# Performance work log

Measured on AMD Instinct MI355X. Metric: run time of the kernel, lower is better.

## Reference

```python
import jax, jax.numpy as jnp
import numpy as np

NOISE_STD = 0.05
ALPHA = 0.2
B, T, I, H, O = 64, 1000, 16, 512, 8


def setup_inputs() -> dict:
    key = jax.random.key(0)
    ks = jax.random.split(key, 5)
    x = jax.random.normal(ks[0], (B, T, I), dtype=jnp.float32)
    noise = jax.random.normal(ks[1], (B, T, H), dtype=jnp.float32)
    # parameter init mirrors torch: wi ~ N(0,1), wrec ~ N(0, rho/sqrt(H)), wo ~ N(0, 1/H)
    wi = jax.random.normal(ks[2], (I, H), dtype=jnp.float32)
    si = jnp.ones((I,), dtype=jnp.float32)
    wrec = jax.random.normal(ks[3], (H, H), dtype=jnp.float32) * (1.0 / np.sqrt(H))
    wo = jax.random.normal(ks[4], (H, O), dtype=jnp.float32) * (1.0 / H)
    so = jnp.ones((O,), dtype=jnp.float32)
    h0 = jnp.zeros((H,), dtype=jnp.float32)
    return {"x": x, "noise": noise, "wi": wi, "si": si, "wrec": wrec,
            "wo": wo, "so": so, "h0": h0}


def reference(x, noise, wi, si, wrec, wo, so, h0):
    # proxy params: wi_full = (wi.T * si).T ; wo_full = wo * so
    wi_full = si[:, None] * wi            # (I, H)
    wo_full = wo * so                      # (H, O)
    # input projection is time-parallel; hoist out of the scan
    x_proj = jnp.einsum('bti,ih->bth', x, wi_full)  # (B, T, H)

    def step(h, inp):
        xp, nz = inp                       # (B, H) each
        r = jnp.tanh(h)
        h_new = h + NOISE_STD * nz + ALPHA * (-h + r @ wrec.T + xp)
        out_t = jnp.tanh(h_new) @ wo_full  # (B, O)
        return h_new, out_t

    h_init = jnp.broadcast_to(h0, (x.shape[0], h0.shape[0]))
    _, out = jax.lax.scan(step, h_init,
                          (jnp.swapaxes(x_proj, 0, 1), jnp.swapaxes(noise, 0, 1)))
    return jnp.swapaxes(out, 0, 1)         # (B, T, O)
```

## Files before the change

### kernel.cpp

```cpp
#include <hip/hip_runtime.h>

#define BB 64
#define TT 1000
#define II 16
#define HH 512
#define OO 8
#define NOISE_STD 0.05f
#define ALPHA 0.2f

#define NGROUPS 32
#define BPG 2
#define NSLABS 8
#define JS 64
#define NTHREADS 512
#define NBLOCKS (NGROUPS * NSLABS)


__global__ void __launch_bounds__(NTHREADS, 1) rnn_kernel(
    const float* __restrict__ x, const float* __restrict__ noise,
    const float* __restrict__ wi, const float* __restrict__ si,
    const float* __restrict__ wrec, const float* __restrict__ wo,
    const float* __restrict__ so, const float* __restrict__ h0,
    float* __restrict__ out, unsigned long long* rtag)
{
    __shared__ __align__(16) float rlds[2][BPG][HH];
    __shared__ __align__(16) float zpart[NSLABS][BPG][JS];
    __shared__ __align__(16) float xpbuf[2][BPG][JS];

    const int tid  = threadIdx.x;
    const int lane = tid & 63;
    const int wid  = tid >> 6;

    const int xcd  = blockIdx.x & 7;
    const int bidx = blockIdx.x >> 3;
    const int grp  = xcd * 4 + (bidx >> 3);
    const int slab = bidx & 7;
    const int gb   = grp * BPG;
    const int j0   = slab * JS;

    float w_reg[64];
    {
        const float4* wrow = (const float4*)(wrec + (size_t)(j0 + lane) * HH + wid * 64);
        #pragma unroll
        for (int c = 0; c < 16; ++c) {
            float4 v = wrow[c];
            w_reg[4*c+0] = v.x; w_reg[4*c+1] = v.y;
            w_reg[4*c+2] = v.z; w_reg[4*c+3] = v.w;
        }
    }

    float hreg = 0.f;
    if (wid < BPG) hreg = h0[j0 + lane];

    float wiF_r[16];
    if (wid >= 6) {
        #pragma unroll
        for (int i = 0; i < 16; ++i) wiF_r[i] = si[i] * wi[i * HH + j0 + lane];
    }
    float wo_r[8][8];
    if (wid == 4 || wid == 5) {
        float so_[8];
        #pragma unroll
        for (int o = 0; o < 8; ++o) so_[o] = so[o];
        #pragma unroll
        for (int m = 0; m < 8; ++m) {
            const float4* wrow = (const float4*)(wo + (size_t)(lane + 64 * m) * OO);
            float4 wa = wrow[0], wb2 = wrow[1];
            wo_r[m][0] = wa.x  * so_[0]; wo_r[m][1] = wa.y  * so_[1];
            wo_r[m][2] = wa.z  * so_[2]; wo_r[m][3] = wa.w  * so_[3];
            wo_r[m][4] = wb2.x * so_[4]; wo_r[m][5] = wb2.y * so_[5];
            wo_r[m][6] = wb2.z * so_[6]; wo_r[m][7] = wb2.w * so_[7];
        }
    }

    {
        float rv = tanhf(h0[tid]);
        rlds[0][0][tid] = rv;
        rlds[0][1][tid] = rv;
    }
    if (wid >= 6) {
        const int b = wid - 6;
        const float4* xb = (const float4*)(x + ((size_t)(gb + b) * TT + 0) * II);
        float4 x0 = xb[0], x1 = xb[1], x2 = xb[2], x3 = xb[3];
        xpbuf[0][b][lane] =
              x0.x*wiF_r[0]  + x0.y*wiF_r[1]  + x0.z*wiF_r[2]  + x0.w*wiF_r[3]
            + x1.x*wiF_r[4]  + x1.y*wiF_r[5]  + x1.z*wiF_r[6]  + x1.w*wiF_r[7]
            + x2.x*wiF_r[8]  + x2.y*wiF_r[9]  + x2.z*wiF_r[10] + x2.w*wiF_r[11]
            + x3.x*wiF_r[12] + x3.y*wiF_r[13] + x3.z*wiF_r[14] + x3.w*wiF_r[15];
    }
    __syncthreads();

    for (int t = 0; t < TT; ++t) {
        const int par = t & 1;
        const int nxt = (t + 1) & 1;

        float nz = 0.f;
        if (wid < BPG)
            nz = noise[((size_t)(gb + wid) * TT + t) * HH + j0 + lane];

        if (t > 0 && wid != slab) {
            const unsigned long long* s0 =
                rtag + (size_t)par * (BB * HH) + (size_t)gb * HH + wid * 64 + lane;
            unsigned long long v0, v1;
            const unsigned int tg = (unsigned int)t;
            do {
                v0 = __hip_atomic_load(s0,      __ATOMIC_RELAXED, __HIP_MEMORY_SCOPE_AGENT);
                v1 = __hip_atomic_load(s0 + HH, __ATOMIC_RELAXED, __HIP_MEMORY_SCOPE_AGENT);
            } while ((unsigned int)(v0 >> 32) != tg || (unsigned int)(v1 >> 32) != tg);
            rlds[par][0][wid * 64 + lane] = __uint_as_float((unsigned int)v0);
            rlds[par][1][wid * 64 + lane] = __uint_as_float((unsigned int)v1);
        }

        float a0 = 0.f, a1 = 0.f;
        {
            const float4* r0p = (const float4*)&rlds[par][0][wid * 64];
            const float4* r1p = (const float4*)&rlds[par][1][wid * 64];
            #pragma unroll
            for (int c = 0; c < 16; ++c) {
                float4 r0 = r0p[c];
                float4 r1 = r1p[c];
                a0 += w_reg[4*c+0]*r0.x + w_reg[4*c+1]*r0.y
                    + w_reg[4*c+2]*r0.z + w_reg[4*c+3]*r0.w;
                a1 += w_reg[4*c+0]*r1.x + w_reg[4*c+1]*r1.y
                    + w_reg[4*c+2]*r1.z + w_reg[4*c+3]*r1.w;
            }
        }
        zpart[wid][0][lane] = a0;
        zpart[wid][1][lane] = a1;
        __syncthreads();

        if (wid < BPG) {
            float z = 0.f;
            #pragma unroll
            for (int k8 = 0; k8 < 8; ++k8) z += zpart[k8][wid][lane];
            float xp = xpbuf[par][wid][lane];
            float hn = hreg + NOISE_STD * nz + ALPHA * (z + xp - hreg);
            hreg = hn;
            float rnew = tanhf(hn);
            unsigned long long pv =
                ((unsigned long long)(unsigned int)(t + 1) << 32)
              | (unsigned long long)__float_as_uint(rnew);
            __hip_atomic_store(rtag + (size_t)nxt * (BB * HH)
                                    + (size_t)(gb + wid) * HH + j0 + lane,
                               pv, __ATOMIC_RELAXED, __HIP_MEMORY_SCOPE_AGENT);
            rlds[nxt][wid][j0 + lane] = rnew;
        } else if (wid == 4 || wid == 5) {
            const int b = wid - 4;
            if (t > 0) {
                float acc0=0.f,acc1=0.f,acc2=0.f,acc3=0.f,
                      acc4=0.f,acc5=0.f,acc6=0.f,acc7=0.f;
                #pragma unroll
                for (int m = 0; m < 8; ++m) {
                    float rv = rlds[par][b][lane + 64 * m];
                    acc0 += rv * wo_r[m][0]; acc1 += rv * wo_r[m][1];
                    acc2 += rv * wo_r[m][2]; acc3 += rv * wo_r[m][3];
                    acc4 += rv * wo_r[m][4]; acc5 += rv * wo_r[m][5];
                    acc6 += rv * wo_r[m][6]; acc7 += rv * wo_r[m][7];
                }
                float res = 0.f;
                #define RED_(A, O) { float v_ = A; \
                    v_ += __shfl_xor(v_, 1);  v_ += __shfl_xor(v_, 2); \
                    v_ += __shfl_xor(v_, 4);  v_ += __shfl_xor(v_, 8); \
                    v_ += __shfl_xor(v_, 16); v_ += __shfl_xor(v_, 32); \
                    if (lane == O) res = v_; }
                RED_(acc0, 0) RED_(acc1, 1) RED_(acc2, 2) RED_(acc3, 3)
                RED_(acc4, 4) RED_(acc5, 5) RED_(acc6, 6) RED_(acc7, 7)
                #undef RED_
                if (lane < 8)
                    out[((size_t)(gb + b) * TT + (t - 1)) * OO + lane] = res;
            }
        } else if (wid >= 6) {
            const int b = wid - 6;
            if (t + 1 < TT) {
                const float4* xb =
                    (const float4*)(x + ((size_t)(gb + b) * TT + (t + 1)) * II);
                float4 x0 = xb[0], x1 = xb[1], x2 = xb[2], x3 = xb[3];
                xpbuf[nxt][b][lane] =
                      x0.x*wiF_r[0]  + x0.y*wiF_r[1]  + x0.z*wiF_r[2]  + x0.w*wiF_r[3]
                    + x1.x*wiF_r[4]  + x1.y*wiF_r[5]  + x1.z*wiF_r[6]  + x1.w*wiF_r[7]
                    + x2.x*wiF_r[8]  + x2.y*wiF_r[9]  + x2.z*wiF_r[10] + x2.w*wiF_r[11]
                    + x3.x*wiF_r[12] + x3.y*wiF_r[13] + x3.z*wiF_r[14] + x3.w*wiF_r[15];
            }
        }
        __syncthreads();
    }

    if (wid != slab) {
        const unsigned long long* s0 =
            rtag + (size_t)gb * HH + wid * 64 + lane;
        unsigned long long v0, v1;
        const unsigned int tg = (unsigned int)TT;
        do {
            v0 = __hip_atomic_load(s0,      __ATOMIC_RELAXED, __HIP_MEMORY_SCOPE_AGENT);
            v1 = __hip_atomic_load(s0 + HH, __ATOMIC_RELAXED, __HIP_MEMORY_SCOPE_AGENT);
        } while ((unsigned int)(v0 >> 32) != tg || (unsigned int)(v1 >> 32) != tg);
        rlds[0][0][wid * 64 + lane] = __uint_as_float((unsigned int)v0);
        rlds[0][1][wid * 64 + lane] = __uint_as_float((unsigned int)v1);
    }
    __syncthreads();
    if (wid == 4 || wid == 5) {
        const int b = wid - 4;
        float acc0=0.f,acc1=0.f,acc2=0.f,acc3=0.f,acc4=0.f,acc5=0.f,acc6=0.f,acc7=0.f;
        #pragma unroll
        for (int m = 0; m < 8; ++m) {
            float rv = rlds[0][b][lane + 64 * m];
            acc0 += rv * wo_r[m][0]; acc1 += rv * wo_r[m][1];
            acc2 += rv * wo_r[m][2]; acc3 += rv * wo_r[m][3];
            acc4 += rv * wo_r[m][4]; acc5 += rv * wo_r[m][5];
            acc6 += rv * wo_r[m][6]; acc7 += rv * wo_r[m][7];
        }
        float res = 0.f;
        #define RED_(A, O) { float v_ = A; \
            v_ += __shfl_xor(v_, 1);  v_ += __shfl_xor(v_, 2); \
            v_ += __shfl_xor(v_, 4);  v_ += __shfl_xor(v_, 8); \
            v_ += __shfl_xor(v_, 16); v_ += __shfl_xor(v_, 32); \
            if (lane == O) res = v_; }
        RED_(acc0, 0) RED_(acc1, 1) RED_(acc2, 2) RED_(acc3, 3)
        RED_(acc4, 4) RED_(acc5, 5) RED_(acc6, 6) RED_(acc7, 7)
        #undef RED_
        if (lane < 8)
            out[((size_t)(gb + b) * TT + (TT - 1)) * OO + lane] = res;
    }
}

extern "C" void kernel_launch(void* const* d_in, const int* in_sizes, int n_in,
                              void* d_out, int out_size, void* d_ws, size_t ws_size,
                              hipStream_t stream) {
    const float* x     = (const float*)d_in[0];
    const float* noise = (const float*)d_in[1];
    const float* wi    = (const float*)d_in[2];
    const float* si    = (const float*)d_in[3];
    const float* wrec  = (const float*)d_in[4];
    const float* wo    = (const float*)d_in[5];
    const float* so    = (const float*)d_in[6];
    const float* h0    = (const float*)d_in[7];
    float* out = (float*)d_out;
    unsigned long long* rtag = (unsigned long long*)d_ws;

    (void)in_sizes; (void)n_in; (void)out_size; (void)ws_size;

    void* args[] = {(void*)&x, (void*)&noise, (void*)&wi, (void*)&si,
                    (void*)&wrec, (void*)&wo, (void*)&so, (void*)&h0,
                    (void*)&out, (void*)&rtag};
    hipLaunchCooperativeKernel((void*)rnn_kernel, dim3(NBLOCKS), dim3(NTHREADS),
                               args, 0, stream);
}
```

Baseline: 2.083 ms.

## Broadcast recurrent state via readlane and drop the per-step trailing barrier

Each wave now pulls its 64-element slice of the tanh state from the global tagged buffer, including its own slab. It keeps that slice in registers and computes the mat-vec by broadcasting lanes with readlane instead of reading float4s from LDS. The partial-sum buffer is double-buffered by step parity, which lets the second __syncthreads at the end of each timestep be removed. The aim is to cut LDS traffic and one block barrier per step on the serial critical path. In exchange, every wave must also spin on its own slab's global store, and 128 readlanes per step go through scalar registers.

```diff
diff --git a/kernel.cpp b/kernel.cpp
--- a/kernel.cpp
+++ b/kernel.cpp
@@ -24,7 +24,7 @@
     float* __restrict__ out, unsigned long long* rtag)
 {
     __shared__ __align__(16) float rlds[2][BPG][HH];
-    __shared__ __align__(16) float zpart[NSLABS][BPG][JS];
+    __shared__ __align__(16) float zpart[2][NSLABS][BPG][JS];
     __shared__ __align__(16) float xpbuf[2][BPG][JS];
 
     const int tid  = threadIdx.x;
@@ -73,10 +73,13 @@
         }
     }
 
+    unsigned int rb0, rb1;
     {
-        float rv = tanhf(h0[tid]);
-        rlds[0][0][tid] = rv;
-        rlds[0][1][tid] = rv;
+        float rv = tanhf(h0[wid * 64 + lane]);
+        rb0 = __float_as_uint(rv);
+        rb1 = rb0;
+        rlds[0][0][wid * 64 + lane] = rv;
+        rlds[0][1][wid * 64 + lane] = rv;
     }
     if (wid >= 6) {
         const int b = wid - 6;
@@ -98,7 +101,7 @@
         if (wid < BPG)
             nz = noise[((size_t)(gb + wid) * TT + t) * HH + j0 + lane];
 
-        if (t > 0 && wid != slab) {
+        if (t > 0) {
             const unsigned long long* s0 =
                 rtag + (size_t)par * (BB * HH) + (size_t)gb * HH + wid * 64 + lane;
             unsigned long long v0, v1;
@@ -107,32 +110,28 @@
                 v0 = __hip_atomic_load(s0,      __ATOMIC_RELAXED, __HIP_MEMORY_SCOPE_AGENT);
                 v1 = __hip_atomic_load(s0 + HH, __ATOMIC_RELAXED, __HIP_MEMORY_SCOPE_AGENT);
             } while ((unsigned int)(v0 >> 32) != tg || (unsigned int)(v1 >> 32) != tg);
-            rlds[par][0][wid * 64 + lane] = __uint_as_float((unsigned int)v0);
-            rlds[par][1][wid * 64 + lane] = __uint_as_float((unsigned int)v1);
+            rb0 = (unsigned int)v0;
+            rb1 = (unsigned int)v1;
+            rlds[par][0][wid * 64 + lane] = __uint_as_float(rb0);
+            rlds[par][1][wid * 64 + lane] = __uint_as_float(rb1);
         }
 
         float a0 = 0.f, a1 = 0.f;
-        {
-            const float4* r0p = (const float4*)&rlds[par][0][wid * 64];
-            const float4* r1p = (const float4*)&rlds[par][1][wid * 64];
-            #pragma unroll
-            for (int c = 0; c < 16; ++c) {
-                float4 r0 = r0p[c];
-                float4 r1 = r1p[c];
-                a0 += w_reg[4*c+0]*r0.x + w_reg[4*c+1]*r0.y
-                    + w_reg[4*c+2]*r0.z + w_reg[4*c+3]*r0.w;
-                a1 += w_reg[4*c+0]*r1.x + w_reg[4*c+1]*r1.y
-                    + w_reg[4*c+2]*r1.z + w_reg[4*c+3]*r1.w;
-            }
-        }
-        zpart[wid][0][lane] = a0;
-        zpart[wid][1][lane] = a1;
+        #pragma unroll
+        for (int c = 0; c < 64; ++c) {
+            float r0 = __uint_as_float(__builtin_amdgcn_readlane(rb0, c));
+            float r1 = __uint_as_float(__builtin_amdgcn_readlane(rb1, c));
+            a0 += w_reg[c] * r0;
+            a1 += w_reg[c] * r1;
+        }
+        zpart[par][wid][0][lane] = a0;
+        zpart[par][wid][1][lane] = a1;
         __syncthreads();
 
         if (wid < BPG) {
             float z = 0.f;
             #pragma unroll
-            for (int k8 = 0; k8 < 8; ++k8) z += zpart[k8][wid][lane];
+            for (int k8 = 0; k8 < 8; ++k8) z += zpart[par][k8][wid][lane];
             float xp = xpbuf[par][wid][lane];
             float hn = hreg + NOISE_STD * nz + ALPHA * (z + xp - hreg);
             hreg = hn;
@@ -143,7 +142,6 @@
             __hip_atomic_store(rtag + (size_t)nxt * (BB * HH)
                                     + (size_t)(gb + wid) * HH + j0 + lane,
                                pv, __ATOMIC_RELAXED, __HIP_MEMORY_SCOPE_AGENT);
-            rlds[nxt][wid][j0 + lane] = rnew;
         } else if (wid == 4 || wid == 5) {
             const int b = wid - 4;
             if (t > 0) {
@@ -182,10 +180,9 @@
                     + x3.x*wiF_r[12] + x3.y*wiF_r[13] + x3.z*wiF_r[14] + x3.w*wiF_r[15];
             }
         }
-        __syncthreads();
-    }
-
-    if (wid != slab) {
+    }
+
+    {
         const unsigned long long* s0 =
             rtag + (size_t)gb * HH + wid * 64 + lane;
         unsigned long long v0, v1;
```

Result: faster. 1.992 ms (-4.4%).
